# Kernel tuning notes

Hardware: AMD Instinct MI355X
Metric: run time of the kernel (lower is better)

The kernel has to match this reference:

```python
import jax, jax.numpy as jnp
import numpy as np

N, E = 50000, 800000
IN, HID, OUT = 256, 128, 128


def setup_inputs() -> dict:
    key = jax.random.key(0)
    ks = jax.random.split(key, 6)
    x = jax.random.normal(ks[0], (N, IN), dtype=jnp.float32)
    edge_index = jax.random.randint(ks[1], (2, E), 0, N, dtype=jnp.int32)
    # xavier_normal-ish scales (exact init values irrelevant for correctness baseline)
    W1 = jax.random.normal(ks[2], (IN, HID), dtype=jnp.float32) * (1.414 / np.sqrt(IN))
    att_src = jax.random.normal(ks[3], (HID,), dtype=jnp.float32) * 0.1
    att_dst = jax.random.normal(ks[4], (HID,), dtype=jnp.float32) * 0.1
    W2 = jax.random.normal(ks[5], (HID, OUT), dtype=jnp.float32) * (1.414 / np.sqrt(HID))
    return {"x": x, "edge_index": edge_index, "W1": W1,
            "att_src": att_src, "att_dst": att_dst, "W2": W2}


def _gat_layer(x, edge_index, W, a_src, a_dst):
    """GATConv(heads=1, concat=False, add_self_loops=False, dropout=0), attention=True."""
    n = x.shape[0]
    src, dst = edge_index[0], edge_index[1]  # message x_j = h[src], grouped by index = dst
    h = x @ W                                 # (N, C)
    e_src = h @ a_src                         # (N,) per-node attention logits
    e_dst = h @ a_dst                         # (N,)
    # per-edge: sigmoid(alpha_j + alpha_i), then scatter-softmax over dst neighborhoods
    alpha = jax.nn.sigmoid(e_src[src] + e_dst[dst])             # (E,)
    m = jax.ops.segment_max(alpha, dst, num_segments=n)          # stable softmax max
    ex = jnp.exp(alpha - m[dst])
    denom = jax.ops.segment_sum(ex, dst, num_segments=n)
    w = ex / denom[dst]                                          # (E,)
    # scatter-add aggregation of weighted source features; heads=1 so mean over heads is identity
    return jax.ops.segment_sum(h[src] * w[:, None], dst, num_segments=n)  # (N, C)


def reference(x, edge_index, W1, att_src, att_dst, W2):
    h1 = jax.nn.elu(_gat_layer(x, edge_index, W1, att_src, att_dst))
    # conv2 called with attention=False: mm(h1, W2).view(N,1,C).mean(1) == plain linear
    return h1 @ W2
```

## Files before the change

kernel.cpp:

```cpp
#include <hip/hip_runtime.h>
#include <hip/hip_bf16.h>

#define N_NODES 50000
#define N_EDGES 800000
#define DIN 256
#define DHID 128
#define DOUT 128
#define NBUCK 196
#define BINBLK 256
#define EPB 3125
#define BINIT 13

typedef __attribute__((ext_vector_type(8))) short bf16x8;
typedef __attribute__((ext_vector_type(4))) float f32x4;

__device__ inline unsigned short f2b(float f) {
    __hip_bfloat16 b = __float2bfloat16(f);
    return *reinterpret_cast<unsigned short*>(&b);
}

__global__ __launch_bounds__(256) void convW_kernel(
    const float* __restrict__ W1, const float* __restrict__ W2,
    unsigned short* __restrict__ W1t, unsigned short* __restrict__ W2t)
{
    int i = blockIdx.x * 256 + threadIdx.x;
    if (i < DIN * DHID) {
        int n = i >> 8, k = i & 255;
        W1t[i] = f2b(W1[k * DHID + n]);
    } else {
        int j = i - DIN * DHID;
        int n = j >> 7, k = j & 127;
        W2t[j] = f2b(W2[k * DOUT + n]);
    }
}

__global__ __launch_bounds__(256) void gemm1_mfma(
    const float* __restrict__ x,
    const unsigned short* __restrict__ W1t,
    const float* __restrict__ att_src,
    const float* __restrict__ att_dst,
    unsigned short* __restrict__ hb,
    float* __restrict__ es,
    float* __restrict__ ed)
{
    __shared__ unsigned short W1s[DHID * DIN];

    const int tid = threadIdx.x;
    const int wave = tid >> 6, lane = tid & 63;
    const int row0 = blockIdx.x * 64 + wave * 16;
    const int m = lane & 15, q = lane >> 4;

    {
        const float4* src = (const float4*)W1t;
        float4* dst = (float4*)W1s;
        #pragma unroll
        for (int i = 0; i < 16; ++i)
            dst[tid + i * 256] = src[tid + i * 256];
    }
    __syncthreads();

    int r  = row0 + m;
    int rc = (r < N_NODES) ? r : 0;

    f32x4 acc[8];
    #pragma unroll
    for (int t = 0; t < 8; ++t) acc[t] = (f32x4){0.f, 0.f, 0.f, 0.f};

    const float* xr = x + (size_t)rc * DIN + q * 8;
    const short* wp = (const short*)W1s + q * 8;

    #pragma unroll
    for (int kt = 0; kt < 8; ++kt) {
        float4 f0 = *(const float4*)(xr + kt * 32);
        float4 f1 = *(const float4*)(xr + kt * 32 + 4);
        bf16x8 a;
        a[0] = (short)f2b(f0.x); a[1] = (short)f2b(f0.y);
        a[2] = (short)f2b(f0.z); a[3] = (short)f2b(f0.w);
        a[4] = (short)f2b(f1.x); a[5] = (short)f2b(f1.y);
        a[6] = (short)f2b(f1.z); a[7] = (short)f2b(f1.w);
        #pragma unroll
        for (int t = 0; t < 8; ++t) {
            bf16x8 b = *(const bf16x8*)(wp + (t * 16 + m) * DIN + kt * 32);
            acc[t] = __builtin_amdgcn_mfma_f32_16x16x32_bf16(a, b, acc[t], 0, 0, 0);
        }
    }

    #pragma unroll
    for (int reg = 0; reg < 4; ++reg) {
        int rr = row0 + q * 4 + reg;
        if (rr < N_NODES) {
            #pragma unroll
            for (int t = 0; t < 8; ++t)
                hb[(size_t)rr * DHID + t * 16 + m] = f2b(acc[t][reg]);
        }
    }

    float esr[4] = {0.f, 0.f, 0.f, 0.f}, edr[4] = {0.f, 0.f, 0.f, 0.f};
    #pragma unroll
    for (int t = 0; t < 8; ++t) {
        float as = att_src[t * 16 + m];
        float ad = att_dst[t * 16 + m];
        #pragma unroll
        for (int reg = 0; reg < 4; ++reg) {
            esr[reg] += acc[t][reg] * as;
            edr[reg] += acc[t][reg] * ad;
        }
    }
    #pragma unroll
    for (int off = 8; off; off >>= 1)
        #pragma unroll
        for (int reg = 0; reg < 4; ++reg) {
            esr[reg] += __shfl_xor(esr[reg], off);
            edr[reg] += __shfl_xor(edr[reg], off);
        }
    if (m == 0) {
        #pragma unroll
        for (int reg = 0; reg < 4; ++reg) {
            int rr = row0 + q * 4 + reg;
            if (rr < N_NODES) { es[rr] = esr[reg]; ed[rr] = edr[reg]; }
        }
    }
}

__global__ __launch_bounds__(256) void lhist_kernel(
    const int* __restrict__ ei, int* __restrict__ blockHist)
{
    __shared__ int h[NBUCK];
    const int t = threadIdx.x, blk = blockIdx.x;
    if (t < NBUCK) h[t] = 0;
    __syncthreads();
    const int base = blk * EPB;
    #pragma unroll 1
    for (int it = 0; it < BINIT; ++it) {
        int e = base + it * 256 + t;
        if (e < base + EPB)
            atomicAdd(&h[ei[N_EDGES + e] >> 8], 1);
    }
    __syncthreads();
    if (t < NBUCK) blockHist[t * 256 + blk] = h[t];
}

__global__ __launch_bounds__(256) void blocksum_kernel(
    const int* __restrict__ in, int* __restrict__ blockSums)
{
    __shared__ int ws[4];
    int t = threadIdx.x;
    int v = in[blockIdx.x * 256 + t];
    #pragma unroll
    for (int off = 32; off; off >>= 1) v += __shfl_down(v, off);
    if ((t & 63) == 0) ws[t >> 6] = v;
    __syncthreads();
    if (t == 0) blockSums[blockIdx.x] = ws[0] + ws[1] + ws[2] + ws[3];
}

__global__ __launch_bounds__(256) void scanb_kernel(
    const int* __restrict__ blockSums, int* __restrict__ blockOffsets)
{
    __shared__ int s[256];
    int t = threadIdx.x;
    int v = (t < NBUCK) ? blockSums[t] : 0;
    s[t] = v;
    __syncthreads();
    #pragma unroll
    for (int off = 1; off < 256; off <<= 1) {
        int u = (t >= off) ? s[t - off] : 0;
        __syncthreads();
        s[t] += u;
        __syncthreads();
    }
    if (t < NBUCK) blockOffsets[t] = s[t] - v;
}

__global__ __launch_bounds__(256) void scanc_kernel(
    const int* __restrict__ in, const int* __restrict__ blockOffsets,
    int* __restrict__ outScan)
{
    __shared__ int s[256];
    int t = threadIdx.x;
    int i = blockIdx.x * 256 + t;
    int c = in[i];
    s[t] = c;
    __syncthreads();
    #pragma unroll
    for (int off = 1; off < 256; off <<= 1) {
        int u = (t >= off) ? s[t - off] : 0;
        __syncthreads();
        s[t] += u;
        __syncthreads();
    }
    outScan[i] = blockOffsets[blockIdx.x] + s[t] - c;
}

__global__ __launch_bounds__(256) void binpass_kernel(
    const int* __restrict__ ei,
    const float* __restrict__ es,
    const float* __restrict__ ed,
    const int* __restrict__ matrixScan,
    int2* __restrict__ binned)
{
    __shared__ int lcur[NBUCK];
    const int t = threadIdx.x, blk = blockIdx.x;
    if (t < NBUCK) lcur[t] = matrixScan[t * 256 + blk];
    __syncthreads();
    const int base = blk * EPB;
    #pragma unroll 1
    for (int it = 0; it < BINIT; ++it) {
        int e = base + it * 256 + t;
        if (e < base + EPB) {
            int s = ei[e];
            int d = ei[N_EDGES + e];
            float a  = es[s] + ed[d];
            float sg = 1.f / (1.f + __expf(-a));
            float w  = __expf(sg);
            int pos = atomicAdd(&lcur[d >> 8], 1);
            binned[pos] = make_int2(s | ((d & 255) << 16), __float_as_int(w));
        }
    }
}

__global__ __launch_bounds__(256) void sortpass_kernel(
    const int2* __restrict__ binned,
    const int* __restrict__ matrixScan,
    int2* __restrict__ sortedSW,
    int* __restrict__ offset,
    int* __restrict__ count)
{
    __shared__ int lhist[256], lscan[256], lcur[256];
    const int t = threadIdx.x, b = blockIdx.x;
    const int start = matrixScan[b * 256];
    const int end   = (b == NBUCK - 1) ? N_EDGES : matrixScan[(b + 1) * 256];
    const int cnt   = end - start;

    lhist[t] = 0;
    __syncthreads();
    for (int i = t; i < cnt; i += 256)
        atomicAdd(&lhist[(binned[start + i].x >> 16) & 255], 1);
    __syncthreads();

    int v = lhist[t];
    lscan[t] = v;
    __syncthreads();
    #pragma unroll
    for (int off = 1; off < 256; off <<= 1) {
        int u = (t >= off) ? lscan[t - off] : 0;
        __syncthreads();
        lscan[t] += u;
        __syncthreads();
    }
    int excl = lscan[t] - v;

    int node = (b << 8) + t;
    if (node < N_NODES) { offset[node] = start + excl; count[node] = v; }
    lcur[t] = excl;
    __syncthreads();

    for (int i = t; i < cnt; i += 256) {
        int2 ent = binned[start + i];
        int dlow = (ent.x >> 16) & 255;
        int pos = atomicAdd(&lcur[dlow], 1);
        sortedSW[start + pos] = make_int2(ent.x & 0xFFFF, ent.y);
    }
}

__global__ __launch_bounds__(256) void agg_kernel(
    const int2* __restrict__ sortedSW,
    const int* __restrict__ offset,
    const int* __restrict__ count,
    const unsigned short* __restrict__ hb,
    float* __restrict__ agg)
{
    int node = (blockIdx.x * 256 + threadIdx.x) >> 6;
    int lane = threadIdx.x & 63;
    if (node >= N_NODES) return;

    int beg = offset[node];
    int deg = count[node];

    float2 acc = make_float2(0.f, 0.f);
    float wsum = 0.f;

    for (int base = 0; base < deg; base += 64) {
        int cnt = min(64, deg - base);
        int2 sw = (lane < cnt) ? sortedSW[beg + base + lane] : make_int2(0, 0);

        float wl = __uint_as_float((unsigned)sw.y);
        #pragma unroll
        for (int o = 32; o; o >>= 1) wl += __shfl_xor(wl, o);
        wsum += wl;

        int j = 0;
        for (; j + 8 <= cnt; j += 8) {
            int s0 = __builtin_amdgcn_readlane(sw.x, j + 0);
            int s1 = __builtin_amdgcn_readlane(sw.x, j + 1);
            int s2 = __builtin_amdgcn_readlane(sw.x, j + 2);
            int s3 = __builtin_amdgcn_readlane(sw.x, j + 3);
            int s4 = __builtin_amdgcn_readlane(sw.x, j + 4);
            int s5 = __builtin_amdgcn_readlane(sw.x, j + 5);
            int s6 = __builtin_amdgcn_readlane(sw.x, j + 6);
            int s7 = __builtin_amdgcn_readlane(sw.x, j + 7);
            unsigned u0 = *(const unsigned*)(hb + (size_t)s0 * DHID + 2 * lane);
            unsigned u1 = *(const unsigned*)(hb + (size_t)s1 * DHID + 2 * lane);
            unsigned u2 = *(const unsigned*)(hb + (size_t)s2 * DHID + 2 * lane);
            unsigned u3 = *(const unsigned*)(hb + (size_t)s3 * DHID + 2 * lane);
            unsigned u4 = *(const unsigned*)(hb + (size_t)s4 * DHID + 2 * lane);
            unsigned u5 = *(const unsigned*)(hb + (size_t)s5 * DHID + 2 * lane);
            unsigned u6 = *(const unsigned*)(hb + (size_t)s6 * DHID + 2 * lane);
            unsigned u7 = *(const unsigned*)(hb + (size_t)s7 * DHID + 2 * lane);
            float w0 = __uint_as_float((unsigned)__builtin_amdgcn_readlane(sw.y, j + 0));
            float w1 = __uint_as_float((unsigned)__builtin_amdgcn_readlane(sw.y, j + 1));
            float w2 = __uint_as_float((unsigned)__builtin_amdgcn_readlane(sw.y, j + 2));
            float w3 = __uint_as_float((unsigned)__builtin_amdgcn_readlane(sw.y, j + 3));
            float w4 = __uint_as_float((unsigned)__builtin_amdgcn_readlane(sw.y, j + 4));
            float w5 = __uint_as_float((unsigned)__builtin_amdgcn_readlane(sw.y, j + 5));
            float w6 = __uint_as_float((unsigned)__builtin_amdgcn_readlane(sw.y, j + 6));
            float w7 = __uint_as_float((unsigned)__builtin_amdgcn_readlane(sw.y, j + 7));
            acc.x += w0 * __uint_as_float(u0 << 16);
            acc.y += w0 * __uint_as_float(u0 & 0xffff0000u);
            acc.x += w1 * __uint_as_float(u1 << 16);
            acc.y += w1 * __uint_as_float(u1 & 0xffff0000u);
            acc.x += w2 * __uint_as_float(u2 << 16);
            acc.y += w2 * __uint_as_float(u2 & 0xffff0000u);
            acc.x += w3 * __uint_as_float(u3 << 16);
            acc.y += w3 * __uint_as_float(u3 & 0xffff0000u);
            acc.x += w4 * __uint_as_float(u4 << 16);
            acc.y += w4 * __uint_as_float(u4 & 0xffff0000u);
            acc.x += w5 * __uint_as_float(u5 << 16);
            acc.y += w5 * __uint_as_float(u5 & 0xffff0000u);
            acc.x += w6 * __uint_as_float(u6 << 16);
            acc.y += w6 * __uint_as_float(u6 & 0xffff0000u);
            acc.x += w7 * __uint_as_float(u7 << 16);
            acc.y += w7 * __uint_as_float(u7 & 0xffff0000u);
        }
        for (; j < cnt; ++j) {
            int   sj = __builtin_amdgcn_readlane(sw.x, j);
            float wj = __uint_as_float((unsigned)__builtin_amdgcn_readlane(sw.y, j));
            unsigned u = *(const unsigned*)(hb + (size_t)sj * DHID + 2 * lane);
            acc.x += wj * __uint_as_float(u << 16);
            acc.y += wj * __uint_as_float(u & 0xffff0000u);
        }
    }
    float inv = (deg > 0) ? 1.f / wsum : 0.f;
    ((float2*)(agg + (size_t)node * DHID))[lane] = make_float2(acc.x * inv, acc.y * inv);
}

__global__ __launch_bounds__(256) void gemm2_mfma(
    const float* __restrict__ agg,
    const unsigned short* __restrict__ W2t,
    float* __restrict__ out)
{
    __shared__ unsigned short W2s[DOUT * DHID];

    const int tid = threadIdx.x;
    const int wave = tid >> 6, lane = tid & 63;
    const int row0 = blockIdx.x * 64 + wave * 16;
    const int m = lane & 15, q = lane >> 4;

    {
        const float4* src = (const float4*)W2t;
        float4* dst = (float4*)W2s;
        #pragma unroll
        for (int i = 0; i < 8; ++i)
            dst[tid + i * 256] = src[tid + i * 256];
    }
    __syncthreads();

    int r  = row0 + m;
    int rc = (r < N_NODES) ? r : 0;

    f32x4 acc[8];
    #pragma unroll
    for (int t = 0; t < 8; ++t) acc[t] = (f32x4){0.f, 0.f, 0.f, 0.f};

    const float* ar = agg + (size_t)rc * DHID + q * 8;
    const short* wp = (const short*)W2s + q * 8;

    #pragma unroll
    for (int kt = 0; kt < 4; ++kt) {
        float4 f0 = *(const float4*)(ar + kt * 32);
        float4 f1 = *(const float4*)(ar + kt * 32 + 4);
        float e0 = f0.x > 0.f ? f0.x : (__expf(f0.x) - 1.f);
        float e1 = f0.y > 0.f ? f0.y : (__expf(f0.y) - 1.f);
        float e2 = f0.z > 0.f ? f0.z : (__expf(f0.z) - 1.f);
        float e3 = f0.w > 0.f ? f0.w : (__expf(f0.w) - 1.f);
        float e4 = f1.x > 0.f ? f1.x : (__expf(f1.x) - 1.f);
        float e5 = f1.y > 0.f ? f1.y : (__expf(f1.y) - 1.f);
        float e6 = f1.z > 0.f ? f1.z : (__expf(f1.z) - 1.f);
        float e7 = f1.w > 0.f ? f1.w : (__expf(f1.w) - 1.f);
        bf16x8 a;
        a[0] = (short)f2b(e0); a[1] = (short)f2b(e1);
        a[2] = (short)f2b(e2); a[3] = (short)f2b(e3);
        a[4] = (short)f2b(e4); a[5] = (short)f2b(e5);
        a[6] = (short)f2b(e6); a[7] = (short)f2b(e7);
        #pragma unroll
        for (int t = 0; t < 8; ++t) {
            bf16x8 b = *(const bf16x8*)(wp + (t * 16 + m) * DHID + kt * 32);
            acc[t] = __builtin_amdgcn_mfma_f32_16x16x32_bf16(a, b, acc[t], 0, 0, 0);
        }
    }

    #pragma unroll
    for (int reg = 0; reg < 4; ++reg) {
        int rr = row0 + q * 4 + reg;
        if (rr < N_NODES) {
            #pragma unroll
            for (int t = 0; t < 8; ++t)
                out[(size_t)rr * DOUT + t * 16 + m] = acc[t][reg];
        }
    }
}

extern "C" void kernel_launch(void* const* d_in, const int* in_sizes, int n_in,
                              void* d_out, int out_size, void* d_ws, size_t ws_size,
                              hipStream_t stream)
{
    const float* x    = (const float*)d_in[0];
    const int*   ei   = (const int*)d_in[1];
    const float* W1   = (const float*)d_in[2];
    const float* asrc = (const float*)d_in[3];
    const float* adst = (const float*)d_in[4];
    const float* W2   = (const float*)d_in[5];
    float*       out  = (float*)d_out;

    char* p = (char*)d_ws;
    unsigned short* hb  = (unsigned short*)p;  p += (size_t)N_NODES * DHID * 2;
    unsigned short* W1t = (unsigned short*)p;  p += (size_t)DHID * DIN * 2;
    unsigned short* W2t = (unsigned short*)p;  p += (size_t)DOUT * DHID * 2;
    float* es     = (float*)p;  p += (size_t)N_NODES * 4;
    float* ed     = (float*)p;  p += (size_t)N_NODES * 4;
    int*   offset = (int*)p;    p += (size_t)N_NODES * 4;
    int*   count  = (int*)p;    p += (size_t)N_NODES * 4;
    int*   blockHist    = (int*)p; p += (size_t)NBUCK * 256 * 4;
    int*   matrixScan   = (int*)p; p += (size_t)NBUCK * 256 * 4;
    int*   blockSums    = (int*)p; p += 256 * 4;
    int*   blockOffsets = (int*)p; p += 256 * 4;
    int2*  binned   = (int2*)p; p += (size_t)N_EDGES * 8;
    int2*  sortedSW = (int2*)p; p += (size_t)N_EDGES * 8;
    float* agg      = (float*)p;

    convW_kernel<<<(DIN * DHID + DHID * DOUT) / 256, 256, 0, stream>>>(W1, W2, W1t, W2t);

    gemm1_mfma<<<(N_NODES + 63) / 64, 256, 0, stream>>>(x, W1t, asrc, adst, hb, es, ed);

    lhist_kernel   <<<BINBLK, 256, 0, stream>>>(ei, blockHist);
    blocksum_kernel<<<NBUCK, 256, 0, stream>>>(blockHist, blockSums);
    scanb_kernel   <<<1, 256, 0, stream>>>(blockSums, blockOffsets);
    scanc_kernel   <<<NBUCK, 256, 0, stream>>>(blockHist, blockOffsets, matrixScan);
    binpass_kernel <<<BINBLK, 256, 0, stream>>>(ei, es, ed, matrixScan, binned);
    sortpass_kernel<<<NBUCK, 256, 0, stream>>>(binned, matrixScan, sortedSW, offset, count);

    agg_kernel<<<(N_NODES * 64 + 255) / 256, 256, 0, stream>>>(
        sortedSW, offset, count, hb, agg);

    gemm2_mfma<<<(N_NODES + 63) / 64, 256, 0, stream>>>(agg, W2t, out);
}
```

Baseline: 197.5 us.

## Fuse scan kernels, move ELU+bf16 pack into aggregation, deepen gather unroll

Result: no change. 195.2 us (-1.2%).

```diff
diff --git a/kernel.cpp b/kernel.cpp
--- a/kernel.cpp
+++ b/kernel.cpp
@@ -123,7 +123,8 @@
 }
 
 __global__ __launch_bounds__(256) void lhist_kernel(
-    const int* __restrict__ ei, int* __restrict__ blockHist)
+    const int* __restrict__ ei, int* __restrict__ blockHist,
+    int* __restrict__ bucketTotals)
 {
     __shared__ int h[NBUCK];
     const int t = threadIdx.x, blk = blockIdx.x;
@@ -137,29 +138,34 @@
             atomicAdd(&h[ei[N_EDGES + e] >> 8], 1);
     }
     __syncthreads();
-    if (t < NBUCK) blockHist[t * 256 + blk] = h[t];
-}
-
-__global__ __launch_bounds__(256) void blocksum_kernel(
-    const int* __restrict__ in, int* __restrict__ blockSums)
-{
-    __shared__ int ws[4];
-    int t = threadIdx.x;
-    int v = in[blockIdx.x * 256 + t];
-    #pragma unroll
-    for (int off = 32; off; off >>= 1) v += __shfl_down(v, off);
-    if ((t & 63) == 0) ws[t >> 6] = v;
-    __syncthreads();
-    if (t == 0) blockSums[blockIdx.x] = ws[0] + ws[1] + ws[2] + ws[3];
-}
-
-__global__ __launch_bounds__(256) void scanb_kernel(
-    const int* __restrict__ blockSums, int* __restrict__ blockOffsets)
-{
+    if (t < NBUCK) {
+        blockHist[t * 256 + blk] = h[t];
+        atomicAdd(&bucketTotals[t], h[t]);
+    }
+}
+
+__global__ __launch_bounds__(256) void scanfused_kernel(
+    const int* __restrict__ bucketTotals,
+    const int* __restrict__ blockHist,
+    int* __restrict__ matrixScan)
+{
+    __shared__ int bs[256];
     __shared__ int s[256];
-    int t = threadIdx.x;
-    int v = (t < NBUCK) ? blockSums[t] : 0;
-    s[t] = v;
+    const int t = threadIdx.x, b = blockIdx.x;
+
+    bs[t] = (t < NBUCK) ? bucketTotals[t] : 0;
+    __syncthreads();
+    #pragma unroll
+    for (int off = 1; off < 256; off <<= 1) {
+        int u = (t >= off) ? bs[t - off] : 0;
+        __syncthreads();
+        bs[t] += u;
+        __syncthreads();
+    }
+    const int base = (b == 0) ? 0 : bs[b - 1];
+
+    int c = blockHist[b * 256 + t];
+    s[t] = c;
     __syncthreads();
     #pragma unroll
     for (int off = 1; off < 256; off <<= 1) {
@@ -168,27 +174,7 @@
         s[t] += u;
         __syncthreads();
     }
-    if (t < NBUCK) blockOffsets[t] = s[t] - v;
-}
-
-__global__ __launch_bounds__(256) void scanc_kernel(
-    const int* __restrict__ in, const int* __restrict__ blockOffsets,
-    int* __restrict__ outScan)
-{
-    __shared__ int s[256];
-    int t = threadIdx.x;
-    int i = blockIdx.x * 256 + t;
-    int c = in[i];
-    s[t] = c;
-    __syncthreads();
-    #pragma unroll
-    for (int off = 1; off < 256; off <<= 1) {
-        int u = (t >= off) ? s[t - off] : 0;
-        __syncthreads();
-        s[t] += u;
-        __syncthreads();
-    }
-    outScan[i] = blockOffsets[blockIdx.x] + s[t] - c;
+    matrixScan[b * 256 + t] = base + s[t] - c;
 }
 
 __global__ __launch_bounds__(256) void binpass_kernel(
@@ -267,7 +253,7 @@
     const int* __restrict__ offset,
     const int* __restrict__ count,
     const unsigned short* __restrict__ hb,
-    float* __restrict__ agg)
+    unsigned int* __restrict__ h1b)
 {
     int node = (blockIdx.x * 256 + threadIdx.x) >> 6;
     int lane = threadIdx.x & 63;
@@ -282,69 +268,51 @@
     for (int base = 0; base < deg; base += 64) {
         int cnt = min(64, deg - base);
         int2 sw = (lane < cnt) ? sortedSW[beg + base + lane] : make_int2(0, 0);
-
-        float wl = __uint_as_float((unsigned)sw.y);
-        #pragma unroll
-        for (int o = 32; o; o >>= 1) wl += __shfl_xor(wl, o);
-        wsum += wl;
-
         int j = 0;
-        for (; j + 8 <= cnt; j += 8) {
-            int s0 = __builtin_amdgcn_readlane(sw.x, j + 0);
-            int s1 = __builtin_amdgcn_readlane(sw.x, j + 1);
-            int s2 = __builtin_amdgcn_readlane(sw.x, j + 2);
-            int s3 = __builtin_amdgcn_readlane(sw.x, j + 3);
-            int s4 = __builtin_amdgcn_readlane(sw.x, j + 4);
-            int s5 = __builtin_amdgcn_readlane(sw.x, j + 5);
-            int s6 = __builtin_amdgcn_readlane(sw.x, j + 6);
-            int s7 = __builtin_amdgcn_readlane(sw.x, j + 7);
-            unsigned u0 = *(const unsigned*)(hb + (size_t)s0 * DHID + 2 * lane);
-            unsigned u1 = *(const unsigned*)(hb + (size_t)s1 * DHID + 2 * lane);
-            unsigned u2 = *(const unsigned*)(hb + (size_t)s2 * DHID + 2 * lane);
-            unsigned u3 = *(const unsigned*)(hb + (size_t)s3 * DHID + 2 * lane);
-            unsigned u4 = *(const unsigned*)(hb + (size_t)s4 * DHID + 2 * lane);
-            unsigned u5 = *(const unsigned*)(hb + (size_t)s5 * DHID + 2 * lane);
-            unsigned u6 = *(const unsigned*)(hb + (size_t)s6 * DHID + 2 * lane);
-            unsigned u7 = *(const unsigned*)(hb + (size_t)s7 * DHID + 2 * lane);
-            float w0 = __uint_as_float((unsigned)__builtin_amdgcn_readlane(sw.y, j + 0));
-            float w1 = __uint_as_float((unsigned)__builtin_amdgcn_readlane(sw.y, j + 1));
-            float w2 = __uint_as_float((unsigned)__builtin_amdgcn_readlane(sw.y, j + 2));
-            float w3 = __uint_as_float((unsigned)__builtin_amdgcn_readlane(sw.y, j + 3));
-            float w4 = __uint_as_float((unsigned)__builtin_amdgcn_readlane(sw.y, j + 4));
-            float w5 = __uint_as_float((unsigned)__builtin_amdgcn_readlane(sw.y, j + 5));
-            float w6 = __uint_as_float((unsigned)__builtin_amdgcn_readlane(sw.y, j + 6));
-            float w7 = __uint_as_float((unsigned)__builtin_amdgcn_readlane(sw.y, j + 7));
-            acc.x += w0 * __uint_as_float(u0 << 16);
-            acc.y += w0 * __uint_as_float(u0 & 0xffff0000u);
-            acc.x += w1 * __uint_as_float(u1 << 16);
-            acc.y += w1 * __uint_as_float(u1 & 0xffff0000u);
-            acc.x += w2 * __uint_as_float(u2 << 16);
-            acc.y += w2 * __uint_as_float(u2 & 0xffff0000u);
-            acc.x += w3 * __uint_as_float(u3 << 16);
-            acc.y += w3 * __uint_as_float(u3 & 0xffff0000u);
-            acc.x += w4 * __uint_as_float(u4 << 16);
-            acc.y += w4 * __uint_as_float(u4 & 0xffff0000u);
-            acc.x += w5 * __uint_as_float(u5 << 16);
-            acc.y += w5 * __uint_as_float(u5 & 0xffff0000u);
-            acc.x += w6 * __uint_as_float(u6 << 16);
-            acc.y += w6 * __uint_as_float(u6 & 0xffff0000u);
-            acc.x += w7 * __uint_as_float(u7 << 16);
-            acc.y += w7 * __uint_as_float(u7 & 0xffff0000u);
-        }
+
+#define TIER(T)                                                                 \
+        for (; j + T <= cnt; j += T) {                                          \
+            unsigned uu[T]; float ww[T];                                        \
+            _Pragma("unroll")                                                   \
+            for (int k = 0; k < T; ++k) {                                       \
+                int s_ = __builtin_amdgcn_readlane(sw.x, j + k);                \
+                uu[k] = *(const unsigned*)(hb + (size_t)s_ * DHID + 2 * lane);  \
+            }                                                                   \
+            _Pragma("unroll")                                                   \
+            for (int k = 0; k < T; ++k)                                         \
+                ww[k] = __uint_as_float(                                        \
+                    (unsigned)__builtin_amdgcn_readlane(sw.y, j + k));          \
+            _Pragma("unroll")                                                   \
+            for (int k = 0; k < T; ++k) {                                       \
+                wsum  += ww[k];                                                 \
+                acc.x += ww[k] * __uint_as_float(uu[k] << 16);                  \
+                acc.y += ww[k] * __uint_as_float(uu[k] & 0xffff0000u);          \
+            }                                                                   \
+        }
+
+        TIER(16)
+        TIER(8)
+        TIER(4)
+#undef TIER
         for (; j < cnt; ++j) {
             int   sj = __builtin_amdgcn_readlane(sw.x, j);
             float wj = __uint_as_float((unsigned)__builtin_amdgcn_readlane(sw.y, j));
             unsigned u = *(const unsigned*)(hb + (size_t)sj * DHID + 2 * lane);
             acc.x += wj * __uint_as_float(u << 16);
             acc.y += wj * __uint_as_float(u & 0xffff0000u);
+            wsum  += wj;
         }
     }
     float inv = (deg > 0) ? 1.f / wsum : 0.f;
-    ((float2*)(agg + (size_t)node * DHID))[lane] = make_float2(acc.x * inv, acc.y * inv);
+    float v0 = acc.x * inv, v1 = acc.y * inv;
+    float e0 = v0 > 0.f ? v0 : (__expf(v0) - 1.f);
+    float e1 = v1 > 0.f ? v1 : (__expf(v1) - 1.f);
+    h1b[(size_t)node * (DHID / 2) + lane] =
+        (unsigned)f2b(e0) | ((unsigned)f2b(e1) << 16);
 }
 
 __global__ __launch_bounds__(256) void gemm2_mfma(
-    const float* __restrict__ agg,
+    const unsigned short* __restrict__ h1b,
     const unsigned short* __restrict__ W2t,
     float* __restrict__ out)
 {
@@ -371,26 +339,12 @@
     #pragma unroll
     for (int t = 0; t < 8; ++t) acc[t] = (f32x4){0.f, 0.f, 0.f, 0.f};
 
-    const float* ar = agg + (size_t)rc * DHID + q * 8;
+    const short* xp = (const short*)h1b + (size_t)rc * DHID + q * 8;
     const short* wp = (const short*)W2s + q * 8;
 
     #pragma unroll
     for (int kt = 0; kt < 4; ++kt) {
-        float4 f0 = *(const float4*)(ar + kt * 32);
-        float4 f1 = *(const float4*)(ar + kt * 32 + 4);
-        float e0 = f0.x > 0.f ? f0.x : (__expf(f0.x) - 1.f);
-        float e1 = f0.y > 0.f ? f0.y : (__expf(f0.y) - 1.f);
-        float e2 = f0.z > 0.f ? f0.z : (__expf(f0.z) - 1.f);
-        float e3 = f0.w > 0.f ? f0.w : (__expf(f0.w) - 1.f);
-        float e4 = f1.x > 0.f ? f1.x : (__expf(f1.x) - 1.f);
-        float e5 = f1.y > 0.f ? f1.y : (__expf(f1.y) - 1.f);
-        float e6 = f1.z > 0.f ? f1.z : (__expf(f1.z) - 1.f);
-        float e7 = f1.w > 0.f ? f1.w : (__expf(f1.w) - 1.f);
-        bf16x8 a;
-        a[0] = (short)f2b(e0); a[1] = (short)f2b(e1);
-        a[2] = (short)f2b(e2); a[3] = (short)f2b(e3);
-        a[4] = (short)f2b(e4); a[5] = (short)f2b(e5);
-        a[6] = (short)f2b(e6); a[7] = (short)f2b(e7);
+        bf16x8 a = *(const bf16x8*)(xp + kt * 32);
         #pragma unroll
         for (int t = 0; t < 8; ++t) {
             bf16x8 b = *(const bf16x8*)(wp + (t * 16 + m) * DHID + kt * 32);
@@ -423,6 +377,7 @@
 
     char* p = (char*)d_ws;
     unsigned short* hb  = (unsigned short*)p;  p += (size_t)N_NODES * DHID * 2;
+    unsigned int*   h1b = (unsigned int*)p;    p += (size_t)N_NODES * DHID * 2;
     unsigned short* W1t = (unsigned short*)p;  p += (size_t)DHID * DIN * 2;
     unsigned short* W2t = (unsigned short*)p;  p += (size_t)DOUT * DHID * 2;
     float* es     = (float*)p;  p += (size_t)N_NODES * 4;
@@ -431,25 +386,23 @@
     int*   count  = (int*)p;    p += (size_t)N_NODES * 4;
     int*   blockHist    = (int*)p; p += (size_t)NBUCK * 256 * 4;
     int*   matrixScan   = (int*)p; p += (size_t)NBUCK * 256 * 4;
-    int*   blockSums    = (int*)p; p += 256 * 4;
-    int*   blockOffsets = (int*)p; p += 256 * 4;
+    int*   bucketTotals = (int*)p; p += 256 * 4;
     int2*  binned   = (int2*)p; p += (size_t)N_EDGES * 8;
     int2*  sortedSW = (int2*)p; p += (size_t)N_EDGES * 8;
-    float* agg      = (float*)p;
+
+    hipMemsetAsync(bucketTotals, 0, NBUCK * sizeof(int), stream);
 
     convW_kernel<<<(DIN * DHID + DHID * DOUT) / 256, 256, 0, stream>>>(W1, W2, W1t, W2t);
 
     gemm1_mfma<<<(N_NODES + 63) / 64, 256, 0, stream>>>(x, W1t, asrc, adst, hb, es, ed);
 
-    lhist_kernel   <<<BINBLK, 256, 0, stream>>>(ei, blockHist);
-    blocksum_kernel<<<NBUCK, 256, 0, stream>>>(blockHist, blockSums);
-    scanb_kernel   <<<1, 256, 0, stream>>>(blockSums, blockOffsets);
-    scanc_kernel   <<<NBUCK, 256, 0, stream>>>(blockHist, blockOffsets, matrixScan);
-    binpass_kernel <<<BINBLK, 256, 0, stream>>>(ei, es, ed, matrixScan, binned);
-    sortpass_kernel<<<NBUCK, 256, 0, stream>>>(binned, matrixScan, sortedSW, offset, count);
+    lhist_kernel    <<<BINBLK, 256, 0, stream>>>(ei, blockHist, bucketTotals);
+    scanfused_kernel<<<NBUCK, 256, 0, stream>>>(bucketTotals, blockHist, matrixScan);
+    binpass_kernel  <<<BINBLK, 256, 0, stream>>>(ei, es, ed, matrixScan, binned);
+    sortpass_kernel <<<NBUCK, 256, 0, stream>>>(binned, matrixScan, sortedSW, offset, count);
 
     agg_kernel<<<(N_NODES * 64 + 255) / 256, 256, 0, stream>>>(
-        sortedSW, offset, count, hb, agg);
-
-    gemm2_mfma<<<(N_NODES + 63) / 64, 256, 0, stream>>>(agg, W2t, out);
-}
+        sortedSW, offset, count, hb, h1b);
+
+    gemm2_mfma<<<(N_NODES + 63) / 64, 256, 0, stream>>>((const unsigned short*)h1b, W2t, out);
+}
```
